# Optimization experiments

Measured on AMD Instinct MI355X. Metric: run time of the kernel, lower is better.

## Reference

```python
import jax, jax.numpy as jnp
import numpy as np

N, E, H = 100000, 3200000, 128


def setup_inputs() -> dict:
    key = jax.random.key(0)
    ks = jax.random.split(key, 12)
    s = 1.0 / np.sqrt(H)
    x = jax.random.normal(ks[0], (N, H), dtype=jnp.float32)
    edge_index = jax.random.randint(ks[1], (2, E), 0, N, dtype=jnp.int64)
    # GatedGraphConv weight: [num_layers=1, H, H] -> single [H, H]
    W = jax.random.normal(ks[2], (H, H), dtype=jnp.float32) * s
    # GRUCell (gate order: r, z, n)
    gru_w_ih = jax.random.normal(ks[3], (3 * H, H), dtype=jnp.float32) * s
    gru_w_hh = jax.random.normal(ks[4], (3 * H, H), dtype=jnp.float32) * s
    gru_b_ih = jax.random.normal(ks[5], (3 * H,), dtype=jnp.float32) * s
    gru_b_hh = jax.random.normal(ks[6], (3 * H,), dtype=jnp.float32) * s
    # LSTM layer 0 (gate order: i, f, g, o)
    lstm_w_ih = jax.random.normal(ks[7], (4 * H, H), dtype=jnp.float32) * s
    lstm_w_hh = jax.random.normal(ks[8], (4 * H, H), dtype=jnp.float32) * s
    lstm_b_ih = jax.random.normal(ks[9], (4 * H,), dtype=jnp.float32) * s
    lstm_b_hh = jax.random.normal(ks[10], (4 * H,), dtype=jnp.float32) * s
    return {
        "x": x, "edge_index": edge_index, "W": W,
        "gru_w_ih": gru_w_ih, "gru_w_hh": gru_w_hh,
        "gru_b_ih": gru_b_ih, "gru_b_hh": gru_b_hh,
        "lstm_w_ih": lstm_w_ih, "lstm_w_hh": lstm_w_hh,
        "lstm_b_ih": lstm_b_ih, "lstm_b_hh": lstm_b_hh,
    }


def _forward(x, edge_index, W, gru_w_ih, gru_w_hh, gru_b_ih, gru_b_hh,
             lstm_w_ih, lstm_w_hh, lstm_b_ih, lstm_b_hh):
    n = x.shape[0]
    src, dst = edge_index[0], edge_index[1]
    # GatedGraphConv, num_layers=1, mean aggregation
    m = x @ W                                   # [N, H]
    msg = m[src]                                # [E, H] gather (memory-bound)
    agg_sum = jax.ops.segment_sum(msg, dst, num_segments=n)
    deg = jax.ops.segment_sum(jnp.ones((src.shape[0],), x.dtype), dst, num_segments=n)
    agg = agg_sum / jnp.maximum(deg, 1.0)[:, None]
    # GRUCell(agg, x): gates r, z, n
    gi = agg @ gru_w_ih.T + gru_b_ih
    gh = x @ gru_w_hh.T + gru_b_hh
    i_r, i_z, i_n = jnp.split(gi, 3, axis=-1)
    h_r, h_z, h_n = jnp.split(gh, 3, axis=-1)
    r = jax.nn.sigmoid(i_r + h_r)
    z = jax.nn.sigmoid(i_z + h_z)
    ng = jnp.tanh(i_n + r * h_n)
    h_conv = (1.0 - z) * ng + z * x             # conv output H_tilde
    # 1-layer LSTM over seq_len=1 with zero initial (H, C)
    gates = h_conv @ lstm_w_ih.T + lstm_b_ih + lstm_b_hh  # h0 = 0
    i_g, f_g, g_g, o_g = jnp.split(gates, 4, axis=-1)
    c = jax.nn.sigmoid(i_g) * jnp.tanh(g_g)
    h_lstm = jax.nn.sigmoid(o_g) * jnp.tanh(c)
    return jax.nn.relu(h_lstm)


def reference(x, edge_index, W, gru_w_ih, gru_w_hh, gru_b_ih, gru_b_hh,
              lstm_w_ih, lstm_w_hh, lstm_b_ih, lstm_b_hh):
    return _forward(x, edge_index, W, gru_w_ih, gru_w_hh, gru_b_ih, gru_b_hh,
                    lstm_w_ih, lstm_w_hh, lstm_b_ih, lstm_b_hh)
```

## Files before the change

### kernel.cpp

```cpp
#include <hip/hip_runtime.h>
#include <math.h>

#define HD 128
#define PB 256
#define SCB 4096

typedef __attribute__((ext_vector_type(8))) short short8;
typedef __attribute__((ext_vector_type(4))) float f32x4;
typedef __attribute__((ext_vector_type(2))) float f32x2;
typedef __attribute__((ext_vector_type(4))) unsigned u32x4;

__device__ __forceinline__ float sigf(float v) { return 1.0f / (1.0f + __expf(-v)); }
__device__ __forceinline__ float tanhf_fast(float v) {
  float e = __expf(2.0f * v);
  return 1.0f - 2.0f / (e + 1.0f);
}

__device__ __forceinline__ unsigned short f2bf(float f) {
  union { float f; unsigned u; } v; v.f = f;
  unsigned r = (v.u + 0x7fffu + ((v.u >> 16) & 1u)) >> 16;
  return (unsigned short)r;
}
__device__ __forceinline__ float bf2f(unsigned short b) {
  union { unsigned u; float f; } v; v.u = ((unsigned)b) << 16;
  return v.f;
}


__global__ __launch_bounds__(256) void bcount_k(const int* __restrict__ ei,
                                                int* __restrict__ bcnt,
                                                int E, int N, int shift, int NB) {
  __shared__ int h[256];
  const int blk = blockIdx.x, tid = threadIdx.x;
  h[tid] = 0;
  __syncthreads();
  int per = (E + PB - 1) / PB;
  int lo = blk * per;
  int hi = (lo + per < E) ? lo + per : E;
  for (int e = lo + tid; e < hi; e += 256) {
    int d = ei[(size_t)E + e];
    if ((unsigned)d >= (unsigned)N) continue;
    atomicAdd(&h[d >> shift], 1);
  }
  __syncthreads();
  if (tid < NB) bcnt[tid * PB + blk] = h[tid];
}

__global__ __launch_bounds__(256) void scan1_k(const int* __restrict__ a,
                                               int* __restrict__ bsums, int total) {
  __shared__ int ts[256];
  int b = blockIdx.x, tid = threadIdx.x;
  int lo = b * SCB + tid * 16;
  int s = 0;
#pragma unroll
  for (int i = 0; i < 16; ++i) {
    int idx = lo + i;
    if (idx < total) s += a[idx];
  }
  ts[tid] = s;
  __syncthreads();
  for (int off = 128; off > 0; off >>= 1) {
    if (tid < off) ts[tid] += ts[tid + off];
    __syncthreads();
  }
  if (tid == 0) bsums[b] = ts[0];
}

__global__ __launch_bounds__(256) void scan2_k(int* __restrict__ bsums, int nb) {
  __shared__ int ts[256];
  int tid = threadIdx.x;
  int v = (tid < nb) ? bsums[tid] : 0;
  ts[tid] = v;
  __syncthreads();
  for (int off = 1; off < 256; off <<= 1) {
    int u = (tid >= off) ? ts[tid - off] : 0;
    __syncthreads();
    ts[tid] += u;
    __syncthreads();
  }
  if (tid < nb) bsums[tid] = ts[tid] - v;
}

__global__ __launch_bounds__(256) void scan3_k(int* __restrict__ a,
                                               const int* __restrict__ bsums,
                                               int total, int nblk) {
  __shared__ int ts[256];
  int b = blockIdx.x, tid = threadIdx.x;
  int lo = b * SCB + tid * 16;
  int pre[16];
  int s = 0;
#pragma unroll
  for (int i = 0; i < 16; ++i) {
    int idx = lo + i;
    int xv = (idx < total) ? a[idx] : 0;
    pre[i] = s;
    s += xv;
  }
  ts[tid] = s;
  __syncthreads();
  for (int off = 1; off < 256; off <<= 1) {
    int u = (tid >= off) ? ts[tid - off] : 0;
    __syncthreads();
    ts[tid] += u;
    __syncthreads();
  }
  int off0 = ts[tid] - s + bsums[b];
#pragma unroll
  for (int i = 0; i < 16; ++i) {
    int idx = lo + i;
    if (idx < total) a[idx] = off0 + pre[i];
  }
  if (b == nblk - 1 && tid == 255) a[total] = off0 + s;
}

__global__ __launch_bounds__(256) void bpart_k(const int* __restrict__ ei,
                                               const int* __restrict__ bstart,
                                               unsigned* __restrict__ ebuf,
                                               int E, int N, int shift, int NB,
                                               int sbits) {
  __shared__ int cur[256];
  const int blk = blockIdx.x, tid = threadIdx.x;
  if (tid < NB) cur[tid] = bstart[tid * PB + blk];
  __syncthreads();
  int per = (E + PB - 1) / PB;
  int lo = blk * per;
  int hi = (lo + per < E) ? lo + per : E;
  const unsigned dmask = (1u << shift) - 1u;
  for (int e = lo + tid; e < hi; e += 256) {
    int s = ei[e];
    int d = ei[(size_t)E + e];
    if ((unsigned)s >= (unsigned)N || (unsigned)d >= (unsigned)N) continue;
    int p = atomicAdd(&cur[d >> shift], 1);
    ebuf[p] = (((unsigned)d & dmask) << sbits) | (unsigned)s;
  }
}

__global__ __launch_bounds__(256) void bfill2_k(const unsigned* __restrict__ ebuf,
                                                const int* __restrict__ bstart,
                                                int* __restrict__ rowstart,
                                                int* __restrict__ csr,
                                                int N, int shift, int NB, int sbits) {
  __shared__ int cnt[2048];
  __shared__ int tsum[256];
  const int b = blockIdx.x, tid = threadIdx.x;
  const int d0 = b << shift;
  int dmax = d0 + (1 << shift);
  if (dmax > N) dmax = N;
  const int nd = dmax - d0;
  const unsigned smask = (1u << sbits) - 1u;
  for (int i = tid; i < nd; i += 256) cnt[i] = 0;
  __syncthreads();
  const int base = bstart[b * PB];
  const int end = bstart[(b + 1) * PB];
  for (int idx = base + tid; idx < end; idx += 256)
    atomicAdd(&cnt[ebuf[idx] >> sbits], 1);
  __syncthreads();
  const int C = (nd + 255) / 256;
  int lo = tid * C;
  int hi = (lo + C < nd) ? lo + C : nd;
  int loc[8];
  int s = 0;
  for (int i = lo; i < hi; ++i) {
    loc[i - lo] = cnt[i];
    s += cnt[i];
  }
  tsum[tid] = s;
  __syncthreads();
  for (int off = 1; off < 256; off <<= 1) {
    int u = (tid >= off) ? tsum[tid - off] : 0;
    __syncthreads();
    tsum[tid] += u;
    __syncthreads();
  }
  int run = tsum[tid] - s + base;
  for (int i = lo; i < hi; ++i) {
    rowstart[d0 + i] = run;
    cnt[i] = run;
    run += loc[i - lo];
  }
  if (b == NB - 1 && tid == 255) rowstart[N] = end;
  __syncthreads();
  for (int idx = base + tid; idx < end; idx += 256) {
    unsigned pk = ebuf[idx];
    int p = atomicAdd(&cnt[pk >> sbits], 1);
    csr[p] = (int)(pk & smask);
  }
}

__global__ __launch_bounds__(256) void prep_k(
    const float* __restrict__ x, unsigned short* __restrict__ xb,
    unsigned* __restrict__ x8,
    const float* __restrict__ gwhh, const float* __restrict__ lwih,
    const float* __restrict__ lbih, const float* __restrict__ lbhh,
    unsigned short* __restrict__ gwhhb, unsigned short* __restrict__ lwb,
    float* __restrict__ lbias,
    const float* __restrict__ W, const float* __restrict__ gwih,
    unsigned short* __restrict__ Bpb, int n4) {
  int t = blockIdx.x * 256 + threadIdx.x;
  if (t < n4) {
    float4 v = reinterpret_cast<const float4*>(x)[t];
    ushort4 o;
    o.x = f2bf(v.x); o.y = f2bf(v.y); o.z = f2bf(v.z); o.w = f2bf(v.w);
    reinterpret_cast<ushort4*>(xb)[t] = o;
    int p8 = 0;
    p8 = __builtin_amdgcn_cvt_pk_fp8_f32(v.x, v.y, p8, false);
    p8 = __builtin_amdgcn_cvt_pk_fp8_f32(v.z, v.w, p8, true);
    x8[t] = (unsigned)p8;
    return;
  }
  t -= n4;
  if (t < 49152) { gwhhb[t] = f2bf(gwhh[t]); return; }
  t -= 49152;
  if (t < 49152) {
    int j = t >> 7, k = t & 127;
    int jm = j < 128 ? j : j + 128;
    lwb[t] = f2bf(lwih[(size_t)jm * 128 + k]);
    return;
  }
  t -= 49152;
  if (t < 384) {
    int jm = t < 128 ? t : t + 128;
    lbias[t] = lbih[jm] + lbhh[jm];
    return;
  }
  t -= 384;
  if (t < 49152) {
    int j = t >> 7, k = t & 127;
    const float4* wr = reinterpret_cast<const float4*>(W + (size_t)k * 128);
    const float4* gr = reinterpret_cast<const float4*>(gwih + (size_t)j * 128);
    float acc = 0.f;
#pragma unroll
    for (int c = 0; c < 32; ++c) {
      float4 a = wr[c], b = gr[c];
      acc += a.x * b.x + a.y * b.y + a.z * b.z + a.w * b.w;
    }
    Bpb[t] = f2bf(acc);
  }
}

__device__ __forceinline__ void accf8(f32x2* acc, uint4 v) {
  acc[0] += __builtin_amdgcn_cvt_pk_f32_fp8((int)v.x, false);
  acc[1] += __builtin_amdgcn_cvt_pk_f32_fp8((int)v.x, true);
  acc[2] += __builtin_amdgcn_cvt_pk_f32_fp8((int)v.y, false);
  acc[3] += __builtin_amdgcn_cvt_pk_f32_fp8((int)v.y, true);
  acc[4] += __builtin_amdgcn_cvt_pk_f32_fp8((int)v.z, false);
  acc[5] += __builtin_amdgcn_cvt_pk_f32_fp8((int)v.z, true);
  acc[6] += __builtin_amdgcn_cvt_pk_f32_fp8((int)v.w, false);
  acc[7] += __builtin_amdgcn_cvt_pk_f32_fp8((int)v.w, true);
}

__global__ __launch_bounds__(256) void gather_f8_k(const int* __restrict__ csr,
                                                   const int* __restrict__ rowstart,
                                                   const unsigned* __restrict__ x8,
                                                   unsigned short* __restrict__ xaggb, int N) {
  int w = (int)(((long long)blockIdx.x * 256 + threadIdx.x) >> 6);
  if (w >= N) return;
  const int lane = threadIdx.x & 63;
  const int sub = lane >> 3, li = lane & 7;
  const int beg = rowstart[w], end = rowstart[w + 1];
  const uint4* x4 = reinterpret_cast<const uint4*>(x8);

  f32x2 acc[8];
#pragma unroll
  for (int i = 0; i < 8; ++i) acc[i] = (f32x2)0.f;

  int j = beg;
  for (; j + 16 <= end; j += 16) {
    int s0 = __builtin_nontemporal_load(&csr[j + sub]);
    int s1 = __builtin_nontemporal_load(&csr[j + 8 + sub]);
    uint4 v0 = x4[(size_t)s0 * 8 + li];
    uint4 v1 = x4[(size_t)s1 * 8 + li];
    accf8(acc, v0);
    accf8(acc, v1);
  }
  for (; j + 8 <= end; j += 8) {
    int s0 = __builtin_nontemporal_load(&csr[j + sub]);
    uint4 v0 = x4[(size_t)s0 * 8 + li];
    accf8(acc, v0);
  }
  int rem = end - j;
  if (sub < rem) {
    int s0 = csr[j + sub];
    uint4 v0 = x4[(size_t)s0 * 8 + li];
    accf8(acc, v0);
  }

  float a16[16];
#pragma unroll
  for (int i = 0; i < 8; ++i) { a16[2 * i] = acc[i].x; a16[2 * i + 1] = acc[i].y; }
#pragma unroll
  for (int i = 0; i < 16; ++i) {
    a16[i] += __shfl_xor(a16[i], 8, 64);
    a16[i] += __shfl_xor(a16[i], 16, 64);
    a16[i] += __shfl_xor(a16[i], 32, 64);
  }

  if (lane < 8) {
    float scale = 1.0f / fmaxf((float)(end - beg), 1.0f);
    u32x4 o1, o2;
    o1.x = (unsigned)f2bf(a16[0] * scale) | ((unsigned)f2bf(a16[1] * scale) << 16);
    o1.y = (unsigned)f2bf(a16[2] * scale) | ((unsigned)f2bf(a16[3] * scale) << 16);
    o1.z = (unsigned)f2bf(a16[4] * scale) | ((unsigned)f2bf(a16[5] * scale) << 16);
    o1.w = (unsigned)f2bf(a16[6] * scale) | ((unsigned)f2bf(a16[7] * scale) << 16);
    o2.x = (unsigned)f2bf(a16[8] * scale) | ((unsigned)f2bf(a16[9] * scale) << 16);
    o2.y = (unsigned)f2bf(a16[10] * scale) | ((unsigned)f2bf(a16[11] * scale) << 16);
    o2.z = (unsigned)f2bf(a16[12] * scale) | ((unsigned)f2bf(a16[13] * scale) << 16);
    o2.w = (unsigned)f2bf(a16[14] * scale) | ((unsigned)f2bf(a16[15] * scale) << 16);
    u32x4* dst = reinterpret_cast<u32x4*>(xaggb + (size_t)w * HD) + li * 2;
    __builtin_nontemporal_store(o1, dst);
    __builtin_nontemporal_store(o2, dst + 1);
  }
}

__global__ __launch_bounds__(256) void gru_fused_k(
    const unsigned short* __restrict__ xaggb, const unsigned short* __restrict__ xb,
    const unsigned short* __restrict__ Bpb, const unsigned short* __restrict__ gwhhb,
    const float* __restrict__ gbih, const float* __restrict__ gbhh,
    unsigned short* __restrict__ hconv, int nrows) {
  __shared__ unsigned short Bsm[96][136];
  const int tid = threadIdx.x;
  const int w = tid >> 6, lane = tid & 63;
  const int q = lane >> 4, r = lane & 15;
  const int row0 = blockIdx.x * 64;

  int arow = row0 + (w << 4) + r;
  int ar = arow < nrows ? arow : nrows - 1;
  const unsigned short* Aa = xaggb + (size_t)ar * HD + q * 8;
  const unsigned short* Ax = xb + (size_t)ar * HD + q * 8;
  short8 a1[4], a2[4];
#pragma unroll
  for (int ks = 0; ks < 4; ++ks) {
    a1[ks] = *reinterpret_cast<const short8*>(Aa + ks * 32);
    a2[ks] = *reinterpret_cast<const short8*>(Ax + ks * 32);
  }

  for (int cg = 0; cg < 4; ++cg) {
    const int c0 = cg * 32;
    f32x4 acc[6][2];
#pragma unroll
    for (int p = 0; p < 6; ++p)
#pragma unroll
      for (int cb = 0; cb < 2; ++cb) acc[p][cb] = (f32x4)0.f;

#pragma unroll
    for (int it = 0; it < 6; ++it) {
      int idx = it * 256 + tid;
      int p = idx >> 9, rem = idx & 511;
      int col = rem >> 4, kq = rem & 15;
      uint4 v = *reinterpret_cast<const uint4*>(
          Bpb + ((size_t)(p * 128 + c0 + col)) * HD + kq * 8);
      *reinterpret_cast<uint4*>(&Bsm[(p << 5) + col][kq * 8]) = v;
    }
    __syncthreads();
#pragma unroll
    for (int ks = 0; ks < 4; ++ks)
#pragma unroll
      for (int p = 0; p < 3; ++p)
#pragma unroll
        for (int cb = 0; cb < 2; ++cb) {
          short8 bf = *reinterpret_cast<const short8*>(
              &Bsm[(p << 5) + cb * 16 + r][ks * 32 + q * 8]);
          acc[p][cb] = __builtin_amdgcn_mfma_f32_16x16x32_bf16(a1[ks], bf, acc[p][cb], 0, 0, 0);
        }
    __syncthreads();

#pragma unroll
    for (int it = 0; it < 6; ++it) {
      int idx = it * 256 + tid;
      int p = idx >> 9, rem = idx & 511;
      int col = rem >> 4, kq = rem & 15;
      uint4 v = *reinterpret_cast<const uint4*>(
          gwhhb + ((size_t)(p * 128 + c0 + col)) * HD + kq * 8);
      *reinterpret_cast<uint4*>(&Bsm[(p << 5) + col][kq * 8]) = v;
    }
    __syncthreads();
#pragma unroll
    for (int ks = 0; ks < 4; ++ks)
#pragma unroll
      for (int p = 0; p < 3; ++p)
#pragma unroll
        for (int cb = 0; cb < 2; ++cb) {
          short8 bf = *reinterpret_cast<const short8*>(
              &Bsm[(p << 5) + cb * 16 + r][ks * 32 + q * 8]);
          acc[3 + p][cb] = __builtin_amdgcn_mfma_f32_16x16x32_bf16(a2[ks], bf, acc[3 + p][cb], 0, 0, 0);
        }

#pragma unroll
    for (int cb = 0; cb < 2; ++cb) {
      int col = c0 + cb * 16 + r;
      float bir = gbih[col], biz = gbih[col + 128], bin = gbih[col + 256];
      float bhr = gbhh[col], bhz = gbhh[col + 128], bhn = gbhh[col + 256];
#pragma unroll
      for (int reg = 0; reg < 4; ++reg) {
        int row = row0 + (w << 4) + q * 4 + reg;
        if (row < nrows) {
          float ir = acc[0][cb][reg] + bir, iz = acc[1][cb][reg] + biz;
          float inn = acc[2][cb][reg] + bin;
          float hr = acc[3][cb][reg] + bhr, hz = acc[4][cb][reg] + bhz;
          float hn = acc[5][cb][reg] + bhn;
          float rr = sigf(ir + hr), zz = sigf(iz + hz);
          float nn = tanhf_fast(inn + rr * hn);
          float xv = bf2f(xb[(size_t)row * HD + col]);
          hconv[(size_t)row * HD + col] = f2bf((1.f - zz) * nn + zz * xv);
        }
      }
    }
    __syncthreads();
  }
}

__global__ __launch_bounds__(256) void lstm_fused_k(
    const unsigned short* __restrict__ hconv, const unsigned short* __restrict__ lwb,
    const float* __restrict__ lbias, float* __restrict__ out, int nrows) {
  __shared__ unsigned short Bsm[96][136];
  const int tid = threadIdx.x;
  const int w = tid >> 6, lane = tid & 63;
  const int q = lane >> 4, r = lane & 15;
  const int row0 = blockIdx.x * 64;

  int arow = row0 + (w << 4) + r;
  int ar = arow < nrows ? arow : nrows - 1;
  const unsigned short* Ap = hconv + (size_t)ar * HD + q * 8;
  short8 hp[4];
#pragma unroll
  for (int ks = 0; ks < 4; ++ks)
    hp[ks] = *reinterpret_cast<const short8*>(Ap + ks * 32);

  for (int cg = 0; cg < 4; ++cg) {
    const int c0 = cg * 32;
    f32x4 acc[3][2];
#pragma unroll
    for (int p = 0; p < 3; ++p)
#pragma unroll
      for (int cb = 0; cb < 2; ++cb) acc[p][cb] = (f32x4)0.f;

#pragma unroll
    for (int it = 0; it < 6; ++it) {
      int idx = it * 256 + tid;
      int p = idx >> 9, rem = idx & 511;
      int col = rem >> 4, kq = rem & 15;
      uint4 v = *reinterpret_cast<const uint4*>(
          lwb + ((size_t)(p * 128 + c0 + col)) * HD + kq * 8);
      *reinterpret_cast<uint4*>(&Bsm[(p << 5) + col][kq * 8]) = v;
    }
    __syncthreads();
#pragma unroll
    for (int ks = 0; ks < 4; ++ks)
#pragma unroll
      for (int p = 0; p < 3; ++p)
#pragma unroll
        for (int cb = 0; cb < 2; ++cb) {
          short8 bf = *reinterpret_cast<const short8*>(
              &Bsm[(p << 5) + cb * 16 + r][ks * 32 + q * 8]);
          acc[p][cb] = __builtin_amdgcn_mfma_f32_16x16x32_bf16(hp[ks], bf, acc[p][cb], 0, 0, 0);
        }

#pragma unroll
    for (int cb = 0; cb < 2; ++cb) {
      int col = c0 + cb * 16 + r;
      float bi = lbias[col], bg = lbias[col + 128], bo = lbias[col + 256];
#pragma unroll
      for (int reg = 0; reg < 4; ++reg) {
        int row = row0 + (w << 4) + q * 4 + reg;
        if (row < nrows) {
          float ig = acc[0][cb][reg] + bi;
          float gg = acc[1][cb][reg] + bg;
          float og = acc[2][cb][reg] + bo;
          float cc = sigf(ig) * tanhf_fast(gg);
          out[(size_t)row * HD + col] = fmaxf(sigf(og) * tanhf_fast(cc), 0.f);
        }
      }
    }
    __syncthreads();
  }
}


extern "C" void kernel_launch(void* const* d_in, const int* in_sizes, int n_in,
                              void* d_out, int out_size, void* d_ws, size_t ws_size,
                              hipStream_t stream) {
  const float* x = (const float*)d_in[0];
  const int* ei = (const int*)d_in[1];
  const float* W = (const float*)d_in[2];
  const float* gw_ih = (const float*)d_in[3];
  const float* gw_hh = (const float*)d_in[4];
  const float* gb_ih = (const float*)d_in[5];
  const float* gb_hh = (const float*)d_in[6];
  const float* lw_ih = (const float*)d_in[7];
  const float* lb_ih = (const float*)d_in[9];
  const float* lb_hh = (const float*)d_in[10];
  float* out = (float*)d_out;

  const int N = in_sizes[0] / HD;
  const int E = in_sizes[1] / 2;
  const size_t nH = (size_t)N * HD;

  int shift = 9;
  while (((N + (1 << shift) - 1) >> shift) > 256) ++shift;
  const int NB = (N + (1 << shift) - 1) >> shift;
  const int sbits = 32 - shift;

  const size_t N4p = (size_t)((N + 1 + 7) & ~7);
  const size_t E4 = (size_t)((E + 3) & ~3);
  const size_t BC = (size_t)NB * PB + 8;
  const int sc_total = NB * PB;
  const int sc_nblk = (sc_total + SCB - 1) / SCB;

  char* p = (char*)d_ws;
  int* rowstart = (int*)p;  p += 4 * N4p;
  int* bcnt = (int*)p;      p += 4 * BC;
  int* bsums = (int*)p;     p += 4 * 64;
  int* csr = (int*)p;       p += 4 * E4;
  size_t sz_eb = 4 * E4, sz_xb = 2 * nH;
  unsigned* ebuf = (unsigned*)p;
  unsigned short* xb = (unsigned short*)p;
  p += (sz_eb > sz_xb ? sz_eb : sz_xb);
  unsigned short* hconv = (unsigned short*)p;  p += 2 * nH;
  unsigned short* Bpb = (unsigned short*)p;    p += 2 * 49152;
  unsigned short* gwhhb = (unsigned short*)p;  p += 2 * 49152;
  unsigned short* lwb = (unsigned short*)p;    p += 2 * 49152;
  float* lbias = (float*)p;                    p += 4 * 384;

  unsigned* x8 = (unsigned*)hconv;

  unsigned short* xaggb = (unsigned short*)d_out;

  dim3 blk(256);
  unsigned rb = (unsigned)((N + 63) / 64);

  bcount_k<<<PB, blk, 0, stream>>>(ei, bcnt, E, N, shift, NB);
  scan1_k<<<sc_nblk, blk, 0, stream>>>(bcnt, bsums, sc_total);
  scan2_k<<<1, blk, 0, stream>>>(bsums, sc_nblk);
  scan3_k<<<sc_nblk, blk, 0, stream>>>(bcnt, bsums, sc_total, sc_nblk);
  bpart_k<<<PB, blk, 0, stream>>>(ei, bcnt, ebuf, E, N, shift, NB, sbits);
  bfill2_k<<<NB, blk, 0, stream>>>(ebuf, bcnt, rowstart, csr, N, shift, NB, sbits);

  int n4 = (int)(nH / 4);
  int prep_total = n4 + 49152 + 49152 + 384 + 49152;
  prep_k<<<(unsigned)((prep_total + 255) / 256), blk, 0, stream>>>(
      x, xb, x8, gw_hh, lw_ih, lb_ih, lb_hh, gwhhb, lwb, lbias, W, gw_ih, Bpb, n4);

  long long gthreads = (long long)N * 64;
  gather_f8_k<<<(unsigned)((gthreads + 255) / 256), blk, 0, stream>>>(
      csr, rowstart, x8, xaggb, N);

  gru_fused_k<<<rb, blk, 0, stream>>>(
      xaggb, xb, Bpb, gwhhb, gb_ih, gb_hh, hconv, N);

  lstm_fused_k<<<rb, blk, 0, stream>>>(hconv, lwb, lbias, out, N);
}
```

Before: 471.2 us.

## Split GRU/LSTM column groups across grid, split prep and gather kernels

The GRU and LSTM fused kernels now give each column group of 32 to its own block through a 2D grid, instead of looping over four column groups inside one block. This raises parallelism and removes the in-loop syncs, but the A tiles are reloaded four times. The prep kernel is split into three launches (x conversion, weight conversion, fused weight product), the gather is split into two half-range launches, and the partition block count PB doubles. The extra launches add overhead with no overlap, since they all run on one stream.

After: 451.9 us. 4.1% less time.

```diff
diff --git a/kernel.cpp b/kernel.cpp
--- a/kernel.cpp
+++ b/kernel.cpp
@@ -2,7 +2,7 @@
 #include <math.h>
 
 #define HD 128
-#define PB 256
+#define PB 512
 #define SCB 4096
 
 typedef __attribute__((ext_vector_type(8))) short short8;
@@ -187,28 +187,28 @@
   }
 }
 
-__global__ __launch_bounds__(256) void prep_k(
-    const float* __restrict__ x, unsigned short* __restrict__ xb,
-    unsigned* __restrict__ x8,
+
+__global__ __launch_bounds__(256) void convx_k(const float* __restrict__ x,
+                                               unsigned short* __restrict__ xb,
+                                               unsigned* __restrict__ x8, int n4) {
+  int t = blockIdx.x * 256 + threadIdx.x;
+  if (t >= n4) return;
+  float4 v = reinterpret_cast<const float4*>(x)[t];
+  ushort4 o;
+  o.x = f2bf(v.x); o.y = f2bf(v.y); o.z = f2bf(v.z); o.w = f2bf(v.w);
+  reinterpret_cast<ushort4*>(xb)[t] = o;
+  int p8 = 0;
+  p8 = __builtin_amdgcn_cvt_pk_fp8_f32(v.x, v.y, p8, false);
+  p8 = __builtin_amdgcn_cvt_pk_fp8_f32(v.z, v.w, p8, true);
+  x8[t] = (unsigned)p8;
+}
+
+__global__ __launch_bounds__(256) void prepw_k(
     const float* __restrict__ gwhh, const float* __restrict__ lwih,
     const float* __restrict__ lbih, const float* __restrict__ lbhh,
     unsigned short* __restrict__ gwhhb, unsigned short* __restrict__ lwb,
-    float* __restrict__ lbias,
-    const float* __restrict__ W, const float* __restrict__ gwih,
-    unsigned short* __restrict__ Bpb, int n4) {
+    float* __restrict__ lbias) {
   int t = blockIdx.x * 256 + threadIdx.x;
-  if (t < n4) {
-    float4 v = reinterpret_cast<const float4*>(x)[t];
-    ushort4 o;
-    o.x = f2bf(v.x); o.y = f2bf(v.y); o.z = f2bf(v.z); o.w = f2bf(v.w);
-    reinterpret_cast<ushort4*>(xb)[t] = o;
-    int p8 = 0;
-    p8 = __builtin_amdgcn_cvt_pk_fp8_f32(v.x, v.y, p8, false);
-    p8 = __builtin_amdgcn_cvt_pk_fp8_f32(v.z, v.w, p8, true);
-    x8[t] = (unsigned)p8;
-    return;
-  }
-  t -= n4;
   if (t < 49152) { gwhhb[t] = f2bf(gwhh[t]); return; }
   t -= 49152;
   if (t < 49152) {
@@ -221,21 +221,24 @@
   if (t < 384) {
     int jm = t < 128 ? t : t + 128;
     lbias[t] = lbih[jm] + lbhh[jm];
-    return;
-  }
-  t -= 384;
-  if (t < 49152) {
-    int j = t >> 7, k = t & 127;
-    const float4* wr = reinterpret_cast<const float4*>(W + (size_t)k * 128);
-    const float4* gr = reinterpret_cast<const float4*>(gwih + (size_t)j * 128);
-    float acc = 0.f;
-#pragma unroll
-    for (int c = 0; c < 32; ++c) {
-      float4 a = wr[c], b = gr[c];
-      acc += a.x * b.x + a.y * b.y + a.z * b.z + a.w * b.w;
-    }
-    Bpb[t] = f2bf(acc);
-  }
+  }
+}
+
+__global__ __launch_bounds__(256) void prepbp_k(const float* __restrict__ W,
+                                                const float* __restrict__ gwih,
+                                                unsigned short* __restrict__ Bpb) {
+  int t = blockIdx.x * 256 + threadIdx.x;
+  if (t >= 49152) return;
+  int j = t >> 7, k = t & 127;
+  const float4* wr = reinterpret_cast<const float4*>(W + (size_t)k * 128);
+  const float4* gr = reinterpret_cast<const float4*>(gwih + (size_t)j * 128);
+  float acc = 0.f;
+#pragma unroll
+  for (int c = 0; c < 32; ++c) {
+    float4 a = wr[c], b = gr[c];
+    acc += a.x * b.x + a.y * b.y + a.z * b.z + a.w * b.w;
+  }
+  Bpb[t] = f2bf(acc);
 }
 
 __device__ __forceinline__ void accf8(f32x2* acc, uint4 v) {
@@ -252,9 +255,10 @@
 __global__ __launch_bounds__(256) void gather_f8_k(const int* __restrict__ csr,
                                                    const int* __restrict__ rowstart,
                                                    const unsigned* __restrict__ x8,
-                                                   unsigned short* __restrict__ xaggb, int N) {
-  int w = (int)(((long long)blockIdx.x * 256 + threadIdx.x) >> 6);
-  if (w >= N) return;
+                                                   unsigned short* __restrict__ xaggb,
+                                                   int row0, int rowend) {
+  int w = row0 + (int)(((long long)blockIdx.x * 256 + threadIdx.x) >> 6);
+  if (w >= rowend) return;
   const int lane = threadIdx.x & 63;
   const int sub = lane >> 3, li = lane & 7;
   const int beg = rowstart[w], end = rowstart[w + 1];
@@ -317,11 +321,12 @@
     const unsigned short* __restrict__ Bpb, const unsigned short* __restrict__ gwhhb,
     const float* __restrict__ gbih, const float* __restrict__ gbhh,
     unsigned short* __restrict__ hconv, int nrows) {
-  __shared__ unsigned short Bsm[96][136];
+  __shared__ unsigned short Bsm[3][32][136];
   const int tid = threadIdx.x;
   const int w = tid >> 6, lane = tid & 63;
   const int q = lane >> 4, r = lane & 15;
-  const int row0 = blockIdx.x * 64;
+  const int row0 = blockIdx.y * 64;
+  const int c0 = blockIdx.x * 32;
 
   int arow = row0 + (w << 4) + r;
   int ar = arow < nrows ? arow : nrows - 1;
@@ -334,89 +339,84 @@
     a2[ks] = *reinterpret_cast<const short8*>(Ax + ks * 32);
   }
 
-  for (int cg = 0; cg < 4; ++cg) {
-    const int c0 = cg * 32;
-    f32x4 acc[6][2];
-#pragma unroll
-    for (int p = 0; p < 6; ++p)
-#pragma unroll
-      for (int cb = 0; cb < 2; ++cb) acc[p][cb] = (f32x4)0.f;
-
-#pragma unroll
-    for (int it = 0; it < 6; ++it) {
-      int idx = it * 256 + tid;
-      int p = idx >> 9, rem = idx & 511;
-      int col = rem >> 4, kq = rem & 15;
-      uint4 v = *reinterpret_cast<const uint4*>(
-          Bpb + ((size_t)(p * 128 + c0 + col)) * HD + kq * 8);
-      *reinterpret_cast<uint4*>(&Bsm[(p << 5) + col][kq * 8]) = v;
-    }
-    __syncthreads();
-#pragma unroll
-    for (int ks = 0; ks < 4; ++ks)
-#pragma unroll
-      for (int p = 0; p < 3; ++p)
-#pragma unroll
-        for (int cb = 0; cb < 2; ++cb) {
-          short8 bf = *reinterpret_cast<const short8*>(
-              &Bsm[(p << 5) + cb * 16 + r][ks * 32 + q * 8]);
-          acc[p][cb] = __builtin_amdgcn_mfma_f32_16x16x32_bf16(a1[ks], bf, acc[p][cb], 0, 0, 0);
-        }
-    __syncthreads();
-
-#pragma unroll
-    for (int it = 0; it < 6; ++it) {
-      int idx = it * 256 + tid;
-      int p = idx >> 9, rem = idx & 511;
-      int col = rem >> 4, kq = rem & 15;
-      uint4 v = *reinterpret_cast<const uint4*>(
-          gwhhb + ((size_t)(p * 128 + c0 + col)) * HD + kq * 8);
-      *reinterpret_cast<uint4*>(&Bsm[(p << 5) + col][kq * 8]) = v;
-    }
-    __syncthreads();
-#pragma unroll
-    for (int ks = 0; ks < 4; ++ks)
-#pragma unroll
-      for (int p = 0; p < 3; ++p)
-#pragma unroll
-        for (int cb = 0; cb < 2; ++cb) {
-          short8 bf = *reinterpret_cast<const short8*>(
-              &Bsm[(p << 5) + cb * 16 + r][ks * 32 + q * 8]);
-          acc[3 + p][cb] = __builtin_amdgcn_mfma_f32_16x16x32_bf16(a2[ks], bf, acc[3 + p][cb], 0, 0, 0);
-        }
-
-#pragma unroll
-    for (int cb = 0; cb < 2; ++cb) {
-      int col = c0 + cb * 16 + r;
-      float bir = gbih[col], biz = gbih[col + 128], bin = gbih[col + 256];
-      float bhr = gbhh[col], bhz = gbhh[col + 128], bhn = gbhh[col + 256];
-#pragma unroll
-      for (int reg = 0; reg < 4; ++reg) {
-        int row = row0 + (w << 4) + q * 4 + reg;
-        if (row < nrows) {
-          float ir = acc[0][cb][reg] + bir, iz = acc[1][cb][reg] + biz;
-          float inn = acc[2][cb][reg] + bin;
-          float hr = acc[3][cb][reg] + bhr, hz = acc[4][cb][reg] + bhz;
-          float hn = acc[5][cb][reg] + bhn;
-          float rr = sigf(ir + hr), zz = sigf(iz + hz);
-          float nn = tanhf_fast(inn + rr * hn);
-          float xv = bf2f(xb[(size_t)row * HD + col]);
-          hconv[(size_t)row * HD + col] = f2bf((1.f - zz) * nn + zz * xv);
-        }
+  f32x4 acc[6][2];
+#pragma unroll
+  for (int p = 0; p < 6; ++p)
+#pragma unroll
+    for (int cb = 0; cb < 2; ++cb) acc[p][cb] = (f32x4)0.f;
+
+#pragma unroll
+  for (int it = 0; it < 6; ++it) {
+    int idx = it * 256 + tid;
+    int p = idx >> 9, rem = idx & 511;
+    int col = rem >> 4, kq = rem & 15;
+    uint4 v = *reinterpret_cast<const uint4*>(
+        Bpb + ((size_t)(p * 128 + c0 + col)) * HD + kq * 8);
+    *reinterpret_cast<uint4*>(&Bsm[p][col][kq * 8]) = v;
+  }
+  __syncthreads();
+#pragma unroll
+  for (int ks = 0; ks < 4; ++ks)
+#pragma unroll
+    for (int p = 0; p < 3; ++p)
+#pragma unroll
+      for (int cb = 0; cb < 2; ++cb) {
+        short8 bf = *reinterpret_cast<const short8*>(&Bsm[p][cb * 16 + r][ks * 32 + q * 8]);
+        acc[p][cb] = __builtin_amdgcn_mfma_f32_16x16x32_bf16(a1[ks], bf, acc[p][cb], 0, 0, 0);
+      }
+  __syncthreads();
+
+#pragma unroll
+  for (int it = 0; it < 6; ++it) {
+    int idx = it * 256 + tid;
+    int p = idx >> 9, rem = idx & 511;
+    int col = rem >> 4, kq = rem & 15;
+    uint4 v = *reinterpret_cast<const uint4*>(
+        gwhhb + ((size_t)(p * 128 + c0 + col)) * HD + kq * 8);
+    *reinterpret_cast<uint4*>(&Bsm[p][col][kq * 8]) = v;
+  }
+  __syncthreads();
+#pragma unroll
+  for (int ks = 0; ks < 4; ++ks)
+#pragma unroll
+    for (int p = 0; p < 3; ++p)
+#pragma unroll
+      for (int cb = 0; cb < 2; ++cb) {
+        short8 bf = *reinterpret_cast<const short8*>(&Bsm[p][cb * 16 + r][ks * 32 + q * 8]);
+        acc[3 + p][cb] = __builtin_amdgcn_mfma_f32_16x16x32_bf16(a2[ks], bf, acc[3 + p][cb], 0, 0, 0);
+      }
+
+#pragma unroll
+  for (int cb = 0; cb < 2; ++cb) {
+    int col = c0 + cb * 16 + r;
+    float bir = gbih[col], biz = gbih[col + 128], bin = gbih[col + 256];
+    float bhr = gbhh[col], bhz = gbhh[col + 128], bhn = gbhh[col + 256];
+#pragma unroll
+    for (int reg = 0; reg < 4; ++reg) {
+      int row = row0 + (w << 4) + q * 4 + reg;
+      if (row < nrows) {
+        float ir = acc[0][cb][reg] + bir, iz = acc[1][cb][reg] + biz;
+        float inn = acc[2][cb][reg] + bin;
+        float hr = acc[3][cb][reg] + bhr, hz = acc[4][cb][reg] + bhz;
+        float hn = acc[5][cb][reg] + bhn;
+        float rr = sigf(ir + hr), zz = sigf(iz + hz);
+        float nn = tanhf_fast(inn + rr * hn);
+        float xv = bf2f(xb[(size_t)row * HD + col]);
+        hconv[(size_t)row * HD + col] = f2bf((1.f - zz) * nn + zz * xv);
       }
     }
-    __syncthreads();
   }
 }
 
 __global__ __launch_bounds__(256) void lstm_fused_k(
     const unsigned short* __restrict__ hconv, const unsigned short* __restrict__ lwb,
     const float* __restrict__ lbias, float* __restrict__ out, int nrows) {
-  __shared__ unsigned short Bsm[96][136];
+  __shared__ unsigned short Bsm[3][32][136];
   const int tid = threadIdx.x;
   const int w = tid >> 6, lane = tid & 63;
   const int q = lane >> 4, r = lane & 15;
-  const int row0 = blockIdx.x * 64;
+  const int row0 = blockIdx.y * 64;
+  const int c0 = blockIdx.x * 32;
 
   int arow = row0 + (w << 4) + r;
   int ar = arow < nrows ? arow : nrows - 1;
@@ -426,52 +426,48 @@
   for (int ks = 0; ks < 4; ++ks)
     hp[ks] = *reinterpret_cast<const short8*>(Ap + ks * 32);
 
-  for (int cg = 0; cg < 4; ++cg) {
-    const int c0 = cg * 32;
-    f32x4 acc[3][2];
+#pragma unroll
+  for (int it = 0; it < 6; ++it) {
+    int idx = it * 256 + tid;
+    int p = idx >> 9, rem = idx & 511;
+    int col = rem >> 4, kq = rem & 15;
+    uint4 v = *reinterpret_cast<const uint4*>(
+        lwb + ((size_t)(p * 128 + c0 + col)) * HD + kq * 8);
+    *reinterpret_cast<uint4*>(&Bsm[p][col][kq * 8]) = v;
+  }
+  __syncthreads();
+
+  f32x4 acc[3][2];
+#pragma unroll
+  for (int p = 0; p < 3; ++p)
+#pragma unroll
+    for (int cb = 0; cb < 2; ++cb) acc[p][cb] = (f32x4)0.f;
+
+#pragma unroll
+  for (int ks = 0; ks < 4; ++ks)
 #pragma unroll
     for (int p = 0; p < 3; ++p)
 #pragma unroll
-      for (int cb = 0; cb < 2; ++cb) acc[p][cb] = (f32x4)0.f;
-
-#pragma unroll
-    for (int it = 0; it < 6; ++it) {
-      int idx = it * 256 + tid;
-      int p = idx >> 9, rem = idx & 511;
-      int col = rem >> 4, kq = rem & 15;
-      uint4 v = *reinterpret_cast<const uint4*>(
-          lwb + ((size_t)(p * 128 + c0 + col)) * HD + kq * 8);
-      *reinterpret_cast<uint4*>(&Bsm[(p << 5) + col][kq * 8]) = v;
-    }
-    __syncthreads();
-#pragma unroll
-    for (int ks = 0; ks < 4; ++ks)
-#pragma unroll
-      for (int p = 0; p < 3; ++p)
-#pragma unroll
-        for (int cb = 0; cb < 2; ++cb) {
-          short8 bf = *reinterpret_cast<const short8*>(
-              &Bsm[(p << 5) + cb * 16 + r][ks * 32 + q * 8]);
-          acc[p][cb] = __builtin_amdgcn_mfma_f32_16x16x32_bf16(hp[ks], bf, acc[p][cb], 0, 0, 0);
-        }
-
-#pragma unroll
-    for (int cb = 0; cb < 2; ++cb) {
-      int col = c0 + cb * 16 + r;
-      float bi = lbias[col], bg = lbias[col + 128], bo = lbias[col + 256];
-#pragma unroll
-      for (int reg = 0; reg < 4; ++reg) {
-        int row = row0 + (w << 4) + q * 4 + reg;
-        if (row < nrows) {
-          float ig = acc[0][cb][reg] + bi;
-          float gg = acc[1][cb][reg] + bg;
-          float og = acc[2][cb][reg] + bo;
-          float cc = sigf(ig) * tanhf_fast(gg);
-          out[(size_t)row * HD + col] = fmaxf(sigf(og) * tanhf_fast(cc), 0.f);
-        }
+      for (int cb = 0; cb < 2; ++cb) {
+        short8 bf = *reinterpret_cast<const short8*>(&Bsm[p][cb * 16 + r][ks * 32 + q * 8]);
+        acc[p][cb] = __builtin_amdgcn_mfma_f32_16x16x32_bf16(hp[ks], bf, acc[p][cb], 0, 0, 0);
+      }
+
+#pragma unroll
+  for (int cb = 0; cb < 2; ++cb) {
+    int col = c0 + cb * 16 + r;
+    float bi = lbias[col], bg = lbias[col + 128], bo = lbias[col + 256];
+#pragma unroll
+    for (int reg = 0; reg < 4; ++reg) {
+      int row = row0 + (w << 4) + q * 4 + reg;
+      if (row < nrows) {
+        float ig = acc[0][cb][reg] + bi;
+        float gg = acc[1][cb][reg] + bg;
+        float og = acc[2][cb][reg] + bo;
+        float cc = sigf(ig) * tanhf_fast(gg);
+        out[(size_t)row * HD + col] = fmaxf(sigf(og) * tanhf_fast(cc), 0.f);
       }
     }
-    __syncthreads();
   }
 }
 
@@ -535,17 +531,23 @@
   bpart_k<<<PB, blk, 0, stream>>>(ei, bcnt, ebuf, E, N, shift, NB, sbits);
   bfill2_k<<<NB, blk, 0, stream>>>(ebuf, bcnt, rowstart, csr, N, shift, NB, sbits);
 
-  int n4 = (int)(nH / 4);
-  int prep_total = n4 + 49152 + 49152 + 384 + 49152;
-  prep_k<<<(unsigned)((prep_total + 255) / 256), blk, 0, stream>>>(
-      x, xb, x8, gw_hh, lw_ih, lb_ih, lb_hh, gwhhb, lwb, lbias, W, gw_ih, Bpb, n4);
-
-  long long gthreads = (long long)N * 64;
-  gather_f8_k<<<(unsigned)((gthreads + 255) / 256), blk, 0, stream>>>(
-      csr, rowstart, x8, xaggb, N);
-
-  gru_fused_k<<<rb, blk, 0, stream>>>(
+  convx_k<<<(unsigned)((nH / 4 + 255) / 256), blk, 0, stream>>>(x, xb, x8, (int)(nH / 4));
+  prepw_k<<<(2 * 49152 + 384 + 255) / 256, blk, 0, stream>>>(
+      gw_hh, lw_ih, lb_ih, lb_hh, gwhhb, lwb, lbias);
+  prepbp_k<<<192, blk, 0, stream>>>(W, gw_ih, Bpb);
+
+  int half = N / 2;
+  {
+    long long gt0 = (long long)half * 64;
+    gather_f8_k<<<(unsigned)((gt0 + 255) / 256), blk, 0, stream>>>(
+        csr, rowstart, x8, xaggb, 0, half);
+    long long gt1 = (long long)(N - half) * 64;
+    gather_f8_k<<<(unsigned)((gt1 + 255) / 256), blk, 0, stream>>>(
+        csr, rowstart, x8, xaggb, half, N);
+  }
+
+  gru_fused_k<<<dim3(4, rb), blk, 0, stream>>>(
       xaggb, xb, Bpb, gwhhb, gb_ih, gb_hh, hconv, N);
 
-  lstm_fused_k<<<rb, blk, 0, stream>>>(hconv, lwb, lbias, out, N);
-}
+  lstm_fused_k<<<dim3(4, rb), blk, 0, stream>>>(hconv, lwb, lbias, out, N);
+}
```
